# Kernel optimization log

Hardware: AMD Instinct MI355X
Metric: run time of the kernel (lower is better)

## Reference

```python
import jax, jax.numpy as jnp
import numpy as np

N = 200_000      # active voxels
INC = 64
OUTC = 96
GRID = 128
EPS = 1e-5


def _build_neighbor_maps():
    """Precompute gather/scatter index maps for the 26 off-center hypercube
    offsets (the 4th kernel dim has size 1, so offsets live in 3D)."""
    rng = np.random.default_rng(0)
    G = GRID ** 3
    lin = rng.choice(G, size=N, replace=False).astype(np.int64)
    z = lin % GRID
    y = (lin // GRID) % GRID
    x = lin // (GRID * GRID)
    lookup = np.full(G, -1, np.int64)
    lookup[lin] = np.arange(N)
    offsets = [(dx, dy, dz) for dx in (-1, 0, 1) for dy in (-1, 0, 1)
               for dz in (-1, 0, 1) if (dx, dy, dz) != (0, 0, 0)]
    pin, pout = [], []
    for dx, dy, dz in offsets:
        nx, ny, nz = x + dx, y + dy, z + dz
        valid = (nx >= 0) & (nx < GRID) & (ny >= 0) & (ny < GRID) & (nz >= 0) & (nz < GRID)
        nlin = (nx * GRID + ny) * GRID + nz
        nb = np.where(valid, lookup[np.clip(nlin, 0, G - 1)], -1)
        m = nb >= 0
        pin.append(np.arange(N)[m])
        pout.append(nb[m])
    pmax = max(len(p) for p in pin)
    in_idx = np.zeros((26, pmax), np.int64)          # pad gathers row 0 (harmless)
    out_idx = np.full((26, pmax), N, np.int64)       # pad scatters to sink row N
    for k, (pi, po) in enumerate(zip(pin, pout)):
        in_idx[k, : len(pi)] = pi
        out_idx[k, : len(po)] = po
    return in_idx, out_idx


def setup_inputs() -> dict:
    in_idx, out_idx = _build_neighbor_maps()
    key = jax.random.key(0)
    k1, k2, k3 = jax.random.split(key, 3)
    std = 1.0 / np.sqrt(INC * 27)
    feats = jax.random.normal(k1, (N, INC), jnp.float32)
    W_center = jax.random.normal(k2, (INC, OUTC), jnp.float32) * std
    W_off = jax.random.normal(k3, (26, INC, OUTC), jnp.float32) * std
    gamma = jnp.ones((OUTC,), jnp.float32)   # bn.weight init to 1.0
    beta = jnp.zeros((OUTC,), jnp.float32)   # bn.bias init to 0.0
    return {"feats": feats, "W_center": W_center, "W_off": W_off,
            "gamma": gamma, "beta": beta,
            "in_idx": jnp.asarray(in_idx), "out_idx": jnp.asarray(out_idx)}


def reference(feats, W_center, W_off, gamma, beta, in_idx, out_idx):
    # --- sparse conv-transpose: gather -> GEMM -> scatter-add ---
    out = feats @ W_center                                   # center offset: identity map, [N, outc]
    gathered = feats[in_idx]                                 # [26, P, inc]
    contrib = jnp.einsum('kpc,kcd->kpd', gathered, W_off)    # [26, P, outc]
    out = jnp.concatenate([out, jnp.zeros((1, OUTC), out.dtype)], axis=0)  # sink row
    out = out.at[out_idx.reshape(-1)].add(contrib.reshape(-1, OUTC))[:N]
    # --- BatchNorm (training-mode batch stats) + ReLU ---
    mean = out.mean(axis=0)
    var = out.var(axis=0)
    y = (out - mean) * jax.lax.rsqrt(var + EPS) * gamma + beta
    return jax.nn.relu(y)
```

## Files before the change

kernel.cpp:

```cpp
#include <hip/hip_runtime.h>


#define N_VOX   200000
#define INC     64
#define OUTC    96
#define NOFF    26
#define MROWS   192
#define NBLK    1042
#define NPAD    200192
#define EPSV    1e-5f

using bf16x8 = __attribute__((ext_vector_type(8))) short;
using f32x4  = __attribute__((ext_vector_type(4))) float;

__device__ inline unsigned short f2bf(float x) {
    union { float f; unsigned u; } v; v.f = x;
    unsigned r = (v.u + 0x7FFFu + ((v.u >> 16) & 1u)) >> 16;
    return (unsigned short)r;
}

__device__ __forceinline__ void gload_lds16(const void* g, void* l) {
    __builtin_amdgcn_global_load_lds(
        (const __attribute__((address_space(1))) void*)g,
        (__attribute__((address_space(3))) void*)l, 16, 0, 0);
}

__global__ void fill_src_kernel(const int* __restrict__ in_idx,
                                const int* __restrict__ out_idx,
                                int P, int* __restrict__ srcmap) {
    int idx = blockIdx.x * blockDim.x + threadIdx.x;
    if (idx >= NOFF * P) return;
    int dst = out_idx[idx];
    if (dst >= N_VOX) return;
    int k = idx / P;
    srcmap[(size_t)k * NPAD + dst] = in_idx[idx];
}

__global__ void wprep_kernel(const float* __restrict__ Wc,
                             const float* __restrict__ Woff,
                             unsigned short* __restrict__ Wb) {
    int t = blockIdx.x * blockDim.x + threadIdx.x;
    if (t >= 27 * 2 * 6 * 64) return;
    int lane = t & 63;
    int g    = t >> 6;
    int ct   = g % 6;
    int s    = (g / 6) % 2;
    int m    = g / 12;
    const float* W = (m == 26) ? Wc : (Woff + (size_t)m * INC * OUTC);
    int k0 = s * 32 + (lane >> 4) * 8;
    int c  = ct * 16 + (lane & 15);
    bf16x8 v;
    #pragma unroll
    for (int e = 0; e < 8; ++e)
        v[e] = (short)f2bf(W[(size_t)(k0 + e) * OUTC + c]);
    *(bf16x8*)(Wb + (size_t)t * 8) = v;
}

__global__ void fcvt_kernel(const float* __restrict__ feats,
                            unsigned short* __restrict__ featsb) {
    int i = blockIdx.x * blockDim.x + threadIdx.x;
    if (i >= N_VOX * INC / 8) return;
    const float4* src = (const float4*)feats + (size_t)i * 2;
    float4 f0 = src[0], f1 = src[1];
    bf16x8 v;
    v[0] = (short)f2bf(f0.x); v[1] = (short)f2bf(f0.y);
    v[2] = (short)f2bf(f0.z); v[3] = (short)f2bf(f0.w);
    v[4] = (short)f2bf(f1.x); v[5] = (short)f2bf(f1.y);
    v[6] = (short)f2bf(f1.z); v[7] = (short)f2bf(f1.w);
    *(bf16x8*)(featsb + (size_t)i * 8) = v;
}

template<int STAGE_BF16>
__global__ __launch_bounds__(256, 3)
void conv_mfma_kernel(const unsigned short* __restrict__ featsb,
                      const unsigned short* __restrict__ Wb,
                      const int* __restrict__ srcmap,
                      float* __restrict__ outf,
                      unsigned short* __restrict__ stg,
                      float* __restrict__ pstats) {
    __shared__ __align__(16) unsigned short Wlds[2][6144];

    const int t     = threadIdx.x;
    const int wid   = t >> 6;
    const int lane  = t & 63;
    const int blk   = blockIdx.x;
    const int rbase = blk * MROWS + wid * 48;
    const int row16 = lane & 15;
    const int kgrp  = lane >> 4;

    f32x4  acc[3][6] = {};
    bf16x8 aC[3][2], aN[3][2];

    #pragma unroll
    for (int i = 0; i < 3; ++i)
        gload_lds16(Wb + (size_t)26 * 6144 + (size_t)(t + 256 * i) * 8,
                    &Wlds[0][(t + 256 * i) * 8]);

    int sm_next = (lane < 48) ? srcmap[rbase + lane] : -1;

    bool has_cur = false;
    #pragma unroll
    for (int rt = 0; rt < 3; ++rt) {
        int row = rbase + rt * 16 + row16;
        int src = row < N_VOX ? row : N_VOX;
        const unsigned short* fr = featsb + (size_t)src * INC + kgrp * 8;
        aC[rt][0] = *(const bf16x8*)fr;
        aC[rt][1] = *(const bf16x8*)(fr + 32);
        has_cur = true;
    }
    has_cur = __ballot(has_cur) != 0ull;
    __syncthreads();

    for (int idx = 0; idx < 27; ++idx) {
        const int buf = idx & 1;

        int sm_next2 = -1;
        if (idx <= 24 && lane < 48)
            sm_next2 = srcmap[(size_t)(idx + 1) * NPAD + rbase + lane];

        bool has_next = false;
        if (idx <= 25) {
            bool any = false;
            #pragma unroll
            for (int rt = 0; rt < 3; ++rt) {
                int src = __shfl(sm_next, rt * 16 + row16);
                bf16x8 g0 = {}, g1 = {};
                if (src >= 0) {
                    const unsigned short* fr = featsb + (size_t)src * INC + kgrp * 8;
                    g0 = *(const bf16x8*)fr;
                    g1 = *(const bf16x8*)(fr + 32);
                    any = true;
                }
                aN[rt][0] = g0; aN[rt][1] = g1;
            }
            has_next = __ballot(any) != 0ull;
            #pragma unroll
            for (int i = 0; i < 3; ++i)
                gload_lds16(Wb + (size_t)idx * 6144 + (size_t)(t + 256 * i) * 8,
                            &Wlds[buf ^ 1][(t + 256 * i) * 8]);
        }

        if (has_cur) {
            const unsigned short* WL = Wlds[buf];
            #pragma unroll
            for (int ct = 0; ct < 6; ++ct) {
                bf16x8 b0 = *(const bf16x8*)&WL[(size_t)ct * 512 + lane * 8];
                bf16x8 b1 = *(const bf16x8*)&WL[(size_t)(6 + ct) * 512 + lane * 8];
                #pragma unroll
                for (int rt = 0; rt < 3; ++rt) {
                    acc[rt][ct] = __builtin_amdgcn_mfma_f32_16x16x32_bf16(aC[rt][0], b0, acc[rt][ct], 0, 0, 0);
                    acc[rt][ct] = __builtin_amdgcn_mfma_f32_16x16x32_bf16(aC[rt][1], b1, acc[rt][ct], 0, 0, 0);
                }
            }
        }
        __syncthreads();

        #pragma unroll
        for (int rt = 0; rt < 3; ++rt) { aC[rt][0] = aN[rt][0]; aC[rt][1] = aN[rt][1]; }
        sm_next = sm_next2;
        has_cur = has_next;
    }

    float s6[6], q6[6];
    #pragma unroll
    for (int ct = 0; ct < 6; ++ct) {
        float s = 0.f, q = 0.f;
        #pragma unroll
        for (int rt = 0; rt < 3; ++rt) {
            f32x4 a = acc[rt][ct];
            s += a[0] + a[1] + a[2] + a[3];
            q += a[0]*a[0] + a[1]*a[1] + a[2]*a[2] + a[3]*a[3];
        }
        s += __shfl_xor(s, 16); q += __shfl_xor(q, 16);
        s += __shfl_xor(s, 32); q += __shfl_xor(q, 32);
        s6[ct] = s; q6[ct] = q;
    }
    float* sred = (float*)Wlds;
    if (lane < 16) {
        #pragma unroll
        for (int ct = 0; ct < 6; ++ct) {
            sred[wid * 96 + ct * 16 + lane]       = s6[ct];
            sred[384 + wid * 96 + ct * 16 + lane] = q6[ct];
        }
    }
    __syncthreads();
    if (t < 96) {
        float s = sred[t] + sred[96 + t] + sred[192 + t] + sred[288 + t];
        pstats[(size_t)t * NBLK + blk] = s;
    } else if (t < 192) {
        int c = t - 96;
        float q = sred[384 + c] + sred[480 + c] + sred[576 + c] + sred[672 + c];
        pstats[(size_t)(96 + c) * NBLK + blk] = q;
    }

    #pragma unroll
    for (int rt = 0; rt < 3; ++rt) {
        #pragma unroll
        for (int ct = 0; ct < 6; ++ct) {
            #pragma unroll
            for (int j = 0; j < 4; ++j) {
                int row = rbase + rt * 16 + kgrp * 4 + j;
                if (row < N_VOX) {
                    if (STAGE_BF16)
                        stg[(size_t)row * OUTC + ct * 16 + row16] = f2bf(acc[rt][ct][j]);
                    else
                        outf[(size_t)row * OUTC + ct * 16 + row16] = acc[rt][ct][j];
                }
            }
        }
    }
}

__global__ void stats_reduce_kernel(const float* __restrict__ pstats,
                                    const float* __restrict__ gamma,
                                    const float* __restrict__ beta,
                                    float* __restrict__ scsh) {
    int c = blockIdx.x;
    int t = threadIdx.x;
    float s = 0.f, q = 0.f;
    for (int i = t; i < NBLK; i += 256) {
        s += pstats[(size_t)c * NBLK + i];
        q += pstats[(size_t)(96 + c) * NBLK + i];
    }
    #pragma unroll
    for (int d = 1; d < 64; d <<= 1) {
        s += __shfl_xor(s, d);
        q += __shfl_xor(q, d);
    }
    __shared__ float rs[4], rq[4];
    if ((t & 63) == 0) { rs[t >> 6] = s; rq[t >> 6] = q; }
    __syncthreads();
    if (t == 0) {
        s = rs[0] + rs[1] + rs[2] + rs[3];
        q = rq[0] + rq[1] + rq[2] + rq[3];
        float inv_n = 1.0f / (float)N_VOX;
        float mean = s * inv_n;
        float var  = q * inv_n - mean * mean;
        float sc   = gamma[c] * rsqrtf(var + EPSV);
        scsh[c]      = sc;
        scsh[96 + c] = beta[c] - mean * sc;
    }
}

__global__ void apply_bn_bf16_kernel(const unsigned short* __restrict__ stg,
                                     float* __restrict__ out,
                                     const float* __restrict__ scsh) {
    __shared__ float sc[OUTC], sh[OUTC];
    int t = threadIdx.x;
    if (t < OUTC) { sc[t] = scsh[t]; sh[t] = scsh[96 + t]; }
    __syncthreads();
    const int total8 = N_VOX * OUTC / 8;
    for (int i = blockIdx.x * blockDim.x + t; i < total8; i += gridDim.x * blockDim.x) {
        bf16x8 v = *(const bf16x8*)(stg + (size_t)i * 8);
        int c = (i % 12) * 8;
        float o[8];
        #pragma unroll
        for (int j = 0; j < 8; ++j) {
            union { unsigned u; float f; } w; w.u = (unsigned)(unsigned short)v[j] << 16;
            o[j] = fmaxf(fmaf(w.f, sc[c + j], sh[c + j]), 0.f);
        }
        float4* dst = (float4*)(out + (size_t)i * 8);
        dst[0] = make_float4(o[0], o[1], o[2], o[3]);
        dst[1] = make_float4(o[4], o[5], o[6], o[7]);
    }
}

__global__ void apply_bn_fp32_kernel(float* __restrict__ out,
                                     const float* __restrict__ scsh) {
    __shared__ float sc[OUTC], sh[OUTC];
    int t = threadIdx.x;
    if (t < OUTC) { sc[t] = scsh[t]; sh[t] = scsh[96 + t]; }
    __syncthreads();
    const int total4 = N_VOX * OUTC / 4;
    for (int i = blockIdx.x * blockDim.x + t; i < total4; i += gridDim.x * blockDim.x) {
        float4 v = ((float4*)out)[i];
        int c = (i * 4) % OUTC;
        v.x = fmaxf(fmaf(v.x, sc[c    ], sh[c    ]), 0.f);
        v.y = fmaxf(fmaf(v.y, sc[c + 1], sh[c + 1]), 0.f);
        v.z = fmaxf(fmaf(v.z, sc[c + 2], sh[c + 2]), 0.f);
        v.w = fmaxf(fmaf(v.w, sc[c + 3], sh[c + 3]), 0.f);
        ((float4*)out)[i] = v;
    }
}

extern "C" void kernel_launch(void* const* d_in, const int* in_sizes, int n_in,
                              void* d_out, int out_size, void* d_ws, size_t ws_size,
                              hipStream_t stream) {
    const float* feats   = (const float*)d_in[0];
    const float* Wc      = (const float*)d_in[1];
    const float* Woff    = (const float*)d_in[2];
    const float* gamma   = (const float*)d_in[3];
    const float* beta    = (const float*)d_in[4];
    const int*   in_idx  = (const int*)d_in[5];
    const int*   out_idx = (const int*)d_in[6];
    const int P = in_sizes[5] / NOFF;

    char* w = (char*)d_ws;
    int* srcmap = (int*)w;                   w += (size_t)NOFF * NPAD * 4;
    unsigned short* Wb = (unsigned short*)w; w += (size_t)27 * 6144 * 2;
    float* pstats = (float*)w;               w += (size_t)192 * NBLK * 4;
    float* scsh = (float*)w;                 w += 256 * 4;
    unsigned short* featsb = (unsigned short*)w;
    w += (size_t)(N_VOX + 1) * INC * 2;
    unsigned short* stg = (unsigned short*)w;
    size_t need_stg = (size_t)(w - (char*)d_ws) + (size_t)N_VOX * OUTC * 2;
    bool use_stg = (ws_size >= need_stg);

    hipMemsetAsync(srcmap, 0xFF, (size_t)NOFF * NPAD * 4, stream);
    hipMemsetAsync(featsb + (size_t)N_VOX * INC, 0, INC * 2, stream);
    fill_src_kernel<<<(NOFF * P + 255) / 256, 256, 0, stream>>>(in_idx, out_idx, P, srcmap);
    wprep_kernel<<<(27 * 2 * 6 * 64 + 255) / 256, 256, 0, stream>>>(Wc, Woff, Wb);
    fcvt_kernel<<<(N_VOX * INC / 8 + 255) / 256, 256, 0, stream>>>(feats, featsb);

    float* out = (float*)d_out;
    if (use_stg) {
        conv_mfma_kernel<1><<<NBLK, 256, 0, stream>>>(featsb, Wb, srcmap, out, stg, pstats);
        stats_reduce_kernel<<<96, 256, 0, stream>>>(pstats, gamma, beta, scsh);
        apply_bn_bf16_kernel<<<2048, 256, 0, stream>>>(stg, out, scsh);
    } else {
        conv_mfma_kernel<0><<<NBLK, 256, 0, stream>>>(featsb, Wb, srcmap, out, stg, pstats);
        stats_reduce_kernel<<<96, 256, 0, stream>>>(pstats, gamma, beta, scsh);
        apply_bn_fp32_kernel<<<2048, 256, 0, stream>>>(out, scsh);
    }
}
```

Baseline: 119.3 us.

## Drop register double-buffered feature gathers, prefetch indices two ahead, raise occupancy

The conv kernel no longer keeps a second set of gathered A-fragments in registers for the next offset. Features are gathered in the same iteration they are used, and only the source-map indices are prefetched two offsets ahead, one per lane, with no shuffles. Freeing those registers lets the launch bounds ask for 4 blocks per SIMD instead of 3, so more waves can hide gather latency. The cost is that each iteration's MFMAs now wait directly on that iteration's feature loads, and latency hiding depends on the extra occupancy.

```diff
diff --git a/kernel.cpp b/kernel.cpp
--- a/kernel.cpp
+++ b/kernel.cpp
@@ -71,7 +71,7 @@
 }
 
 template<int STAGE_BF16>
-__global__ __launch_bounds__(256, 3)
+__global__ __launch_bounds__(256, 4)
 void conv_mfma_kernel(const unsigned short* __restrict__ featsb,
                       const unsigned short* __restrict__ Wb,
                       const int* __restrict__ srcmap,
@@ -89,58 +89,66 @@
     const int kgrp  = lane >> 4;
 
     f32x4  acc[3][6] = {};
-    bf16x8 aC[3][2], aN[3][2];
+    int smA[3], smB[3];
 
     #pragma unroll
     for (int i = 0; i < 3; ++i)
         gload_lds16(Wb + (size_t)26 * 6144 + (size_t)(t + 256 * i) * 8,
                     &Wlds[0][(t + 256 * i) * 8]);
 
-    int sm_next = (lane < 48) ? srcmap[rbase + lane] : -1;
-
-    bool has_cur = false;
     #pragma unroll
     for (int rt = 0; rt < 3; ++rt) {
-        int row = rbase + rt * 16 + row16;
-        int src = row < N_VOX ? row : N_VOX;
-        const unsigned short* fr = featsb + (size_t)src * INC + kgrp * 8;
-        aC[rt][0] = *(const bf16x8*)fr;
-        aC[rt][1] = *(const bf16x8*)(fr + 32);
-        has_cur = true;
-    }
-    has_cur = __ballot(has_cur) != 0ull;
+        smA[rt] = -1;
+        smB[rt] = srcmap[rbase + rt * 16 + row16];
+    }
     __syncthreads();
 
     for (int idx = 0; idx < 27; ++idx) {
         const int buf = idx & 1;
 
-        int sm_next2 = -1;
-        if (idx <= 24 && lane < 48)
-            sm_next2 = srcmap[(size_t)(idx + 1) * NPAD + rbase + lane];
-
-        bool has_next = false;
-        if (idx <= 25) {
+        bf16x8 aC[3][2];
+        int has = 0;
+        if (idx == 0) {
+            #pragma unroll
+            for (int rt = 0; rt < 3; ++rt) {
+                int row = rbase + rt * 16 + row16;
+                int src = row < N_VOX ? row : N_VOX;
+                const unsigned short* fr = featsb + (size_t)src * INC + kgrp * 8;
+                aC[rt][0] = *(const bf16x8*)fr;
+                aC[rt][1] = *(const bf16x8*)(fr + 32);
+            }
+            has = 1;
+        } else {
             bool any = false;
             #pragma unroll
             for (int rt = 0; rt < 3; ++rt) {
-                int src = __shfl(sm_next, rt * 16 + row16);
+                int s = smA[rt];
                 bf16x8 g0 = {}, g1 = {};
-                if (src >= 0) {
-                    const unsigned short* fr = featsb + (size_t)src * INC + kgrp * 8;
+                if (s >= 0) {
+                    const unsigned short* fr = featsb + (size_t)s * INC + kgrp * 8;
                     g0 = *(const bf16x8*)fr;
                     g1 = *(const bf16x8*)(fr + 32);
                     any = true;
                 }
-                aN[rt][0] = g0; aN[rt][1] = g1;
+                aC[rt][0] = g0; aC[rt][1] = g1;
             }
-            has_next = __ballot(any) != 0ull;
+            has = (__ballot(any) != 0ull);
+        }
+
+        if (idx <= 25) {
             #pragma unroll
             for (int i = 0; i < 3; ++i)
                 gload_lds16(Wb + (size_t)idx * 6144 + (size_t)(t + 256 * i) * 8,
                             &Wlds[buf ^ 1][(t + 256 * i) * 8]);
         }
-
-        if (has_cur) {
+        int smN[3];
+        if (idx <= 24) {
+            #pragma unroll
+            for (int rt = 0; rt < 3; ++rt)
+                smN[rt] = srcmap[(size_t)(idx + 1) * NPAD + rbase + rt * 16 + row16];
+        }
+
+        if (has) {
             const unsigned short* WL = Wlds[buf];
             #pragma unroll
             for (int ct = 0; ct < 6; ++ct) {
@@ -156,9 +164,10 @@
         __syncthreads();
 
         #pragma unroll
-        for (int rt = 0; rt < 3; ++rt) { aC[rt][0] = aN[rt][0]; aC[rt][1] = aN[rt][1]; }
-        sm_next = sm_next2;
-        has_cur = has_next;
+        for (int rt = 0; rt < 3; ++rt) {
+            smA[rt] = smB[rt];
+            smB[rt] = (idx <= 24) ? smN[rt] : -1;
+        }
     }
 
     float s6[6], q6[6];
```

Result: slower. 128.5 us (+7.7%).

## Fuse prep kernels and use 4-slot weight ring with halved barriers

Applied to the files above, without the earlier changes.

Merges the feature conversion, source-map fill and weight packing kernels into one launch, with the work selected by block range. In the conv kernel the LDS weight buffer grows from two to four slots so each slot is prefetched two iterations ahead, and the block barrier runs only on odd iterations. This cuts launch overhead and barrier stalls. The cost is more LDS per block, which may reduce occupancy, and it relies on the remaining barriers to order the async LDS loads.

```diff
diff --git a/kernel.cpp b/kernel.cpp
--- a/kernel.cpp
+++ b/kernel.cpp
@@ -25,49 +25,62 @@
         (__attribute__((address_space(3))) void*)l, 16, 0, 0);
 }
 
-__global__ void fill_src_kernel(const int* __restrict__ in_idx,
-                                const int* __restrict__ out_idx,
-                                int P, int* __restrict__ srcmap) {
-    int idx = blockIdx.x * blockDim.x + threadIdx.x;
-    if (idx >= NOFF * P) return;
-    int dst = out_idx[idx];
-    if (dst >= N_VOX) return;
-    int k = idx / P;
-    srcmap[(size_t)k * NPAD + dst] = in_idx[idx];
-}
-
-__global__ void wprep_kernel(const float* __restrict__ Wc,
-                             const float* __restrict__ Woff,
-                             unsigned short* __restrict__ Wb) {
-    int t = blockIdx.x * blockDim.x + threadIdx.x;
-    if (t >= 27 * 2 * 6 * 64) return;
-    int lane = t & 63;
-    int g    = t >> 6;
-    int ct   = g % 6;
-    int s    = (g / 6) % 2;
-    int m    = g / 12;
-    const float* W = (m == 26) ? Wc : (Woff + (size_t)m * INC * OUTC);
-    int k0 = s * 32 + (lane >> 4) * 8;
-    int c  = ct * 16 + (lane & 15);
-    bf16x8 v;
-    #pragma unroll
-    for (int e = 0; e < 8; ++e)
-        v[e] = (short)f2bf(W[(size_t)(k0 + e) * OUTC + c]);
-    *(bf16x8*)(Wb + (size_t)t * 8) = v;
-}
-
-__global__ void fcvt_kernel(const float* __restrict__ feats,
-                            unsigned short* __restrict__ featsb) {
-    int i = blockIdx.x * blockDim.x + threadIdx.x;
-    if (i >= N_VOX * INC / 8) return;
-    const float4* src = (const float4*)feats + (size_t)i * 2;
-    float4 f0 = src[0], f1 = src[1];
-    bf16x8 v;
-    v[0] = (short)f2bf(f0.x); v[1] = (short)f2bf(f0.y);
-    v[2] = (short)f2bf(f0.z); v[3] = (short)f2bf(f0.w);
-    v[4] = (short)f2bf(f1.x); v[5] = (short)f2bf(f1.y);
-    v[6] = (short)f2bf(f1.z); v[7] = (short)f2bf(f1.w);
-    *(bf16x8*)(featsb + (size_t)i * 8) = v;
+__global__ void prep_kernel(const float* __restrict__ feats,
+                            const float* __restrict__ Wc,
+                            const float* __restrict__ Woff,
+                            const int* __restrict__ in_idx,
+                            const int* __restrict__ out_idx,
+                            int P, int fill_blocks,
+                            unsigned short* __restrict__ featsb,
+                            unsigned short* __restrict__ Wb,
+                            int* __restrict__ srcmap) {
+    const int FCVT_BLOCKS = (N_VOX * INC / 8 + 255) / 256;
+    int b = blockIdx.x;
+    int t = threadIdx.x;
+    if (b < FCVT_BLOCKS) {
+        int i = b * 256 + t;
+        if (i < N_VOX * INC / 8) {
+            const float4* src = (const float4*)feats + (size_t)i * 2;
+            float4 f0 = src[0], f1 = src[1];
+            bf16x8 v;
+            v[0] = (short)f2bf(f0.x); v[1] = (short)f2bf(f0.y);
+            v[2] = (short)f2bf(f0.z); v[3] = (short)f2bf(f0.w);
+            v[4] = (short)f2bf(f1.x); v[5] = (short)f2bf(f1.y);
+            v[6] = (short)f2bf(f1.z); v[7] = (short)f2bf(f1.w);
+            *(bf16x8*)(featsb + (size_t)i * 8) = v;
+        }
+        return;
+    }
+    b -= FCVT_BLOCKS;
+    if (b < fill_blocks) {
+        int idx = b * 256 + t;
+        if (idx < NOFF * P) {
+            int dst = out_idx[idx];
+            if (dst < N_VOX) {
+                int k = idx / P;
+                srcmap[(size_t)k * NPAD + dst] = in_idx[idx];
+            }
+        }
+        return;
+    }
+    b -= fill_blocks;
+    {
+        int g = b * 256 + t;
+        if (g >= 27 * 2 * 6 * 64) return;
+        int lane = g & 63;
+        int gg   = g >> 6;
+        int ct   = gg % 6;
+        int s    = (gg / 6) % 2;
+        int m    = gg / 12;
+        const float* W = (m == 26) ? Wc : (Woff + (size_t)m * INC * OUTC);
+        int k0 = s * 32 + (lane >> 4) * 8;
+        int c  = ct * 16 + (lane & 15);
+        bf16x8 v;
+        #pragma unroll
+        for (int e = 0; e < 8; ++e)
+            v[e] = (short)f2bf(W[(size_t)(k0 + e) * OUTC + c]);
+        *(bf16x8*)(Wb + (size_t)g * 8) = v;
+    }
 }
 
 template<int STAGE_BF16>
@@ -78,7 +91,7 @@
                       float* __restrict__ outf,
                       unsigned short* __restrict__ stg,
                       float* __restrict__ pstats) {
-    __shared__ __align__(16) unsigned short Wlds[2][6144];
+    __shared__ __align__(16) unsigned short Wlds[4][6144];
 
     const int t     = threadIdx.x;
     const int wid   = t >> 6;
@@ -95,10 +108,14 @@
     for (int i = 0; i < 3; ++i)
         gload_lds16(Wb + (size_t)26 * 6144 + (size_t)(t + 256 * i) * 8,
                     &Wlds[0][(t + 256 * i) * 8]);
+    #pragma unroll
+    for (int i = 0; i < 3; ++i)
+        gload_lds16(Wb + (size_t)(t + 256 * i) * 8,
+                    &Wlds[1][(t + 256 * i) * 8]);
 
     int sm_next = (lane < 48) ? srcmap[rbase + lane] : -1;
 
-    bool has_cur = false;
+    bool has_cur = true;
     #pragma unroll
     for (int rt = 0; rt < 3; ++rt) {
         int row = rbase + rt * 16 + row16;
@@ -106,14 +123,10 @@
         const unsigned short* fr = featsb + (size_t)src * INC + kgrp * 8;
         aC[rt][0] = *(const bf16x8*)fr;
         aC[rt][1] = *(const bf16x8*)(fr + 32);
-        has_cur = true;
-    }
-    has_cur = __ballot(has_cur) != 0ull;
+    }
     __syncthreads();
 
     for (int idx = 0; idx < 27; ++idx) {
-        const int buf = idx & 1;
-
         int sm_next2 = -1;
         if (idx <= 24 && lane < 48)
             sm_next2 = srcmap[(size_t)(idx + 1) * NPAD + rbase + lane];
@@ -134,14 +147,16 @@
                 aN[rt][0] = g0; aN[rt][1] = g1;
             }
             has_next = __ballot(any) != 0ull;
+        }
+        if (idx <= 24) {
             #pragma unroll
             for (int i = 0; i < 3; ++i)
-                gload_lds16(Wb + (size_t)idx * 6144 + (size_t)(t + 256 * i) * 8,
-                            &Wlds[buf ^ 1][(t + 256 * i) * 8]);
+                gload_lds16(Wb + (size_t)(idx + 1) * 6144 + (size_t)(t + 256 * i) * 8,
+                            &Wlds[(idx + 2) & 3][(t + 256 * i) * 8]);
         }
 
         if (has_cur) {
-            const unsigned short* WL = Wlds[buf];
+            const unsigned short* WL = Wlds[idx & 3];
             #pragma unroll
             for (int ct = 0; ct < 6; ++ct) {
                 bf16x8 b0 = *(const bf16x8*)&WL[(size_t)ct * 512 + lane * 8];
@@ -153,7 +168,8 @@
                 }
             }
         }
-        __syncthreads();
+
+        if (idx & 1) __syncthreads();
 
         #pragma unroll
         for (int rt = 0; rt < 3; ++rt) { aC[rt][0] = aN[rt][0]; aC[rt][1] = aN[rt][1]; }
@@ -308,9 +324,12 @@
 
     hipMemsetAsync(srcmap, 0xFF, (size_t)NOFF * NPAD * 4, stream);
     hipMemsetAsync(featsb + (size_t)N_VOX * INC, 0, INC * 2, stream);
-    fill_src_kernel<<<(NOFF * P + 255) / 256, 256, 0, stream>>>(in_idx, out_idx, P, srcmap);
-    wprep_kernel<<<(27 * 2 * 6 * 64 + 255) / 256, 256, 0, stream>>>(Wc, Woff, Wb);
-    fcvt_kernel<<<(N_VOX * INC / 8 + 255) / 256, 256, 0, stream>>>(feats, featsb);
+
+    const int FCVT_BLOCKS = (N_VOX * INC / 8 + 255) / 256;
+    const int fill_blocks = (NOFF * P + 255) / 256;
+    const int WPREP_BLOCKS = (27 * 2 * 6 * 64 + 255) / 256;
+    prep_kernel<<<FCVT_BLOCKS + fill_blocks + WPREP_BLOCKS, 256, 0, stream>>>(
+        feats, Wc, Woff, in_idx, out_idx, P, fill_blocks, featsb, Wb, srcmap);
 
     float* out = (float*)d_out;
     if (use_stg) {
```

Result: faster. 114.5 us (median of 3 runs) (-4.0%).
